# Optimization experiments

Hardware: AMD Instinct MI355X
Metric: run time of the kernel (lower is better)

Reference implementation:

```python
import jax, jax.numpy as jnp
import numpy as np
import math

B, S, H, D = 2, 2048, 12, 64
DIM = H * D
TOTAL = B * S


def setup_inputs() -> dict:
    key = jax.random.key(0)
    ks = jax.random.split(key, 5)
    hidden_states = jax.random.normal(ks[0], (TOTAL, DIM), dtype=jnp.float32)
    Wqkv_w = jax.random.normal(ks[1], (3 * DIM, DIM), dtype=jnp.float32) * (1.0 / math.sqrt(DIM))
    Wqkv_b = jax.random.normal(ks[2], (3 * DIM,), dtype=jnp.float32) * 0.02
    bias = jax.random.normal(ks[3], (B, H, S, S), dtype=jnp.float32) * 0.1
    slopes = jax.random.uniform(ks[4], (H,), dtype=jnp.float32)
    cu_seqlens = jnp.array([0, S, 2 * S], dtype=jnp.int32)
    indices = jnp.arange(TOTAL, dtype=jnp.int64)
    attn_mask = jnp.ones((B, S), dtype=jnp.int32)
    return {"hidden_states": hidden_states, "Wqkv_w": Wqkv_w, "Wqkv_b": Wqkv_b,
            "bias": bias, "slopes": slopes, "cu_seqlens": cu_seqlens,
            "indices": indices, "attn_mask": attn_mask, "max_seqlen": S}


def reference(hidden_states, Wqkv_w, Wqkv_b, bias, slopes, cu_seqlens, indices, attn_mask, max_seqlen):
    total_nnz, dim = hidden_states.shape
    batch = cu_seqlens.shape[0] - 1
    # fused QKV projection (torch Linear: x @ W.T + b)
    qkv = hidden_states @ Wqkv_w.T + Wqkv_b  # (total_nnz, 3*dim)
    # pad_input: scatter unpadded rows into (batch*max_seqlen, 3*dim)
    padded = jnp.zeros((batch * max_seqlen, 3 * dim), dtype=qkv.dtype).at[indices].set(qkv)
    qkv = padded.reshape(batch, max_seqlen, 3, H, D)
    q = qkv[:, :, 0].transpose(0, 2, 1, 3)  # (b, h, s, d)
    k = qkv[:, :, 1].transpose(0, 2, 1, 3)
    v = qkv[:, :, 2].transpose(0, 2, 1, 3)
    scores = jnp.einsum('bhqd,bhkd->bhqk', q, k) / math.sqrt(D)
    scores = scores + bias  # ALiBi (dense bias tensor)
    probs = jax.nn.softmax(scores, axis=-1)  # dropout p=0 -> identity
    attn = jnp.einsum('bhqk,bhkd->bhqd', probs, v)
    attn = attn.transpose(0, 2, 1, 3).reshape(batch * max_seqlen, dim)
    # unpad_input_only: gather valid rows back
    return attn[indices]
```

## Files before the change

kernel.cpp:

```cpp
#include <hip/hip_runtime.h>


typedef __attribute__((ext_vector_type(8))) short short8;
typedef __attribute__((ext_vector_type(4))) float floatx4;
typedef unsigned short u16;
typedef unsigned int u32;

#define LOG2E 1.4426950408889634f

__device__ __forceinline__ u16 f2bf(float f) {
  u32 u = __float_as_uint(f);
  u += 0x7FFFu + ((u >> 16) & 1u);
  return (u16)(u >> 16);
}

typedef const __attribute__((address_space(1))) u32* gp_t;
typedef __attribute__((address_space(3))) u32* lp_t;
__device__ __forceinline__ void async_cp16(const void* g, void* l) {
  __builtin_amdgcn_global_load_lds((gp_t)g, (lp_t)l, 16, 0, 0);
}

__global__ __launch_bounds__(256) void pack_kernel(
    const float* __restrict__ A, const float* __restrict__ W,
    u16* __restrict__ Abf, u16* __restrict__ Wbf) {
  unsigned u = blockIdx.x * 256u + threadIdx.x;
  const unsigned nA = 786432u;
  float4 v;
  u16* dst;
  if (u < nA) { v = ((const float4*)A)[u]; dst = Abf + u * 4; }
  else        { unsigned q = u - nA; v = ((const float4*)W)[q]; dst = Wbf + q * 4; }
  ushort4 o;
  o.x = f2bf(v.x); o.y = f2bf(v.y); o.z = f2bf(v.z); o.w = f2bf(v.w);
  *(ushort4*)dst = o;
}

__global__ __launch_bounds__(256, 3) void qkv_gemm(
    const u16* __restrict__ Abf, const u16* __restrict__ Wbf,
    const float* __restrict__ bq,
    u16* __restrict__ Qb, u16* __restrict__ Kb, u16* __restrict__ Vb) {
  __shared__ __align__(16) char smem[32768];
  char* As0 = smem;
  char* Bs0 = smem + 8192;
  char* As1 = smem + 16384;
  char* Bs1 = smem + 24576;
  const unsigned t = threadIdx.x;
  unsigned orig = blockIdx.y * 18u + blockIdx.x;
  unsigned wg = (orig & 7u) * 72u + (orig >> 3);
  const unsigned nblk = wg % 18u, mblk = wg / 18u;
  const unsigned w = t >> 6, l = t & 63, quad = l >> 4, c = l & 15;
  const unsigned wm = (w >> 1) * 64, wn = (w & 1) * 64;

  floatx4 acc[4][4] = {};

  const unsigned b0 = t, b1 = t + 256u;
  const unsigned r0 = b0 >> 2, ch0 = (b0 & 3u) ^ (r0 & 3u);
  const unsigned r1 = b1 >> 2, ch1 = (b1 & 3u) ^ (r1 & 3u);
  const char* gA0 = (const char*)Abf + (size_t)((mblk * 128 + r0) * 768) * 2 + ch0 * 16;
  const char* gA1 = (const char*)Abf + (size_t)((mblk * 128 + r1) * 768) * 2 + ch1 * 16;
  const char* gB0 = (const char*)Wbf + (size_t)((nblk * 128 + r0) * 768) * 2 + ch0 * 16;
  const char* gB1 = (const char*)Wbf + (size_t)((nblk * 128 + r1) * 768) * 2 + ch1 * 16;

  async_cp16(gA0, As0 + b0 * 16);
  async_cp16(gA1, As0 + b1 * 16);
  async_cp16(gB0, Bs0 + b0 * 16);
  async_cp16(gB1, Bs0 + b1 * 16);
  __syncthreads();

  for (unsigned kt = 0; kt < 24; ++kt) {
    char* Ac = (kt & 1u) ? As1 : As0;
    char* Bc = (kt & 1u) ? Bs1 : Bs0;
    if (kt + 1 < 24) {
      char* An = (kt & 1u) ? As0 : As1;
      char* Bn = (kt & 1u) ? Bs0 : Bs1;
      async_cp16(gA0 + (kt + 1) * 64, An + b0 * 16);
      async_cp16(gA1 + (kt + 1) * 64, An + b1 * 16);
      async_cp16(gB0 + (kt + 1) * 64, Bn + b0 * 16);
      async_cp16(gB1 + (kt + 1) * 64, Bn + b1 * 16);
    }
    short8 af[4], bf[4];
#pragma unroll
    for (int mt = 0; mt < 4; ++mt) {
      unsigned row = wm + mt * 16 + c;
      af[mt] = *(const short8*)(Ac + row * 64 + 16 * (quad ^ (row & 3u)));
    }
#pragma unroll
    for (int nt = 0; nt < 4; ++nt) {
      unsigned row = wn + nt * 16 + c;
      bf[nt] = *(const short8*)(Bc + row * 64 + 16 * (quad ^ (row & 3u)));
    }
#pragma unroll
    for (int mt = 0; mt < 4; ++mt)
#pragma unroll
      for (int nt = 0; nt < 4; ++nt)
        acc[mt][nt] = __builtin_amdgcn_mfma_f32_16x16x32_bf16(af[mt], bf[nt], acc[mt][nt], 0, 0, 0);
    __syncthreads();
  }

  float bqv[4];
#pragma unroll
  for (int nt = 0; nt < 4; ++nt) bqv[nt] = bq[nblk * 128 + wn + nt * 16 + c];
#pragma unroll
  for (int mt = 0; mt < 4; ++mt) {
#pragma unroll
    for (int r = 0; r < 4; ++r) {
      unsigned m = mblk * 128 + wm + mt * 16 + quad * 4 + r;
      unsigned bb = m >> 11, s = m & 2047u;
#pragma unroll
      for (int nt = 0; nt < 4; ++nt) {
        float val = acc[mt][nt][r] + bqv[nt];
        unsigned n = nblk * 128 + wn + nt * 16 + c;
        u16 bv = f2bf(val);
        if (n < 768u) {
          unsigned h = n >> 6, d = n & 63u;
          Qb[(((bb * 12 + h) * 2048 + s) << 6) + d] = bv;
        } else if (n < 1536u) {
          unsigned n2 = n - 768u, h = n2 >> 6, d = n2 & 63u;
          Kb[(((bb * 12 + h) * 2048 + s) << 6) + d] = bv;
        } else {
          unsigned n2 = n - 1536u, h = n2 >> 6, d = n2 & 63u;
          Vb[(((bb * 12 + h) << 6) + d) * 2048 + s] = bv;
        }
      }
    }
  }
}

__global__ __launch_bounds__(256, 6) void attn_kernel(
    const u16* __restrict__ Qb, const u16* __restrict__ Kb,
    const u16* __restrict__ Vb, const float* __restrict__ bias,
    float* __restrict__ Op, float* __restrict__ Mp, float* __restrict__ Lp) {
  __shared__ __align__(16) char smem[20480];
  char* Ks0 = smem;
  char* Ks1 = smem + 4096;
  char* Vs0 = smem + 8192;
  char* Vs1 = smem + 12288;
  char* Ps  = smem + 16384;
  const unsigned t = threadIdx.x;
  unsigned wgid = (blockIdx.x & 7u) * 384u + (blockIdx.x >> 3);
  const unsigned bh = wgid >> 7;
  const unsigned rem = wgid & 127u;
  const unsigned qt = rem >> 2, sp = rem & 3u;
  const unsigned q0 = qt * 64;
  const unsigned w = t >> 6, l = t & 63, quad = l >> 4, c = l & 15;

  const unsigned rK = t >> 3, chK = (t & 7u) ^ (rK & 7u);
  const unsigned rV = t >> 2, chV = (t & 3u) ^ (rV & 3u);

  const char* gK = (const char*)Kb + (size_t)(bh * 2048 + sp * 512 + rK) * 128 + chK * 16;
  const char* gV = (const char*)Vb + (size_t)(bh * 64 + rV) * 4096 + sp * 1024 + chV * 16;
  const float* bias_base = bias + (size_t)(bh * 2048 + q0 + w * 16 + quad * 4) * 2048
                                + sp * 512 + c;
  const unsigned pb = w * 1024u;

  async_cp16(gK, Ks0 + t * 16);
  async_cp16(gV, Vs0 + t * 16);
  short8 aq[2];
  {
    const u16* qrow = Qb + (size_t)(bh * 2048 + q0 + w * 16 + c) * 64 + quad * 8;
    aq[0] = *(const short8*)(qrow);
    aq[1] = *(const short8*)(qrow + 32);
  }
  float bvA[2][4], bvB[2][4];
#pragma unroll
  for (int tt = 0; tt < 2; ++tt)
#pragma unroll
    for (int r = 0; r < 4; ++r)
      bvA[tt][r] = bias_base[(size_t)r * 2048 + tt * 16];
  __syncthreads();

  float mrun[4] = {-1e30f, -1e30f, -1e30f, -1e30f};
  float lrun[4] = {0.f, 0.f, 0.f, 0.f};
  floatx4 oacc[4] = {};

  for (unsigned i = 0; i < 16; ++i) {
    const char* Kc = (i & 1u) ? Ks1 : Ks0;
    const char* Vc = (i & 1u) ? Vs1 : Vs0;

    if (i + 1 < 16) {
      char* Kn = (i & 1u) ? Ks0 : Ks1;
      char* Vn = (i & 1u) ? Vs0 : Vs1;
      async_cp16(gK + (size_t)(i + 1) * 4096, Kn + t * 16);
      async_cp16(gV + (size_t)(i + 1) * 64, Vn + t * 16);
#pragma unroll
      for (int tt = 0; tt < 2; ++tt)
#pragma unroll
        for (int r = 0; r < 4; ++r)
          bvB[tt][r] = bias_base[(size_t)r * 2048 + (i + 1) * 32 + tt * 16];
    }

    floatx4 s4[2] = {};
    __builtin_amdgcn_s_setprio(1);
#pragma unroll
    for (int ds = 0; ds < 2; ++ds)
#pragma unroll
      for (int tt = 0; tt < 2; ++tt) {
        unsigned row = tt * 16 + c;
        short8 kf = *(const short8*)(Kc + row * 128 + 16 * (((unsigned)quad + 4u * ds) ^ (c & 7u)));
        s4[tt] = __builtin_amdgcn_mfma_f32_16x16x32_bf16(aq[ds], kf, s4[tt], 0, 0, 0);
      }
    __builtin_amdgcn_s_setprio(0);

    float alpha[4];
    float pr[2][4];
#pragma unroll
    for (int r = 0; r < 4; ++r) {
      float x0 = fmaf(bvA[0][r], 8.0f, s4[0][r]) * (LOG2E / 8.0f);
      float x1 = fmaf(bvA[1][r], 8.0f, s4[1][r]) * (LOG2E / 8.0f);
      float mx = fmaxf(x0, x1);
      mx = fmaxf(mx, __shfl_xor(mx, 1));
      mx = fmaxf(mx, __shfl_xor(mx, 2));
      mx = fmaxf(mx, __shfl_xor(mx, 4));
      mx = fmaxf(mx, __shfl_xor(mx, 8));
      float mn = fmaxf(mrun[r], mx);
      float a = __builtin_amdgcn_exp2f(mrun[r] - mn);
      mrun[r] = mn;
      float p0 = __builtin_amdgcn_exp2f(x0 - mn);
      float p1 = __builtin_amdgcn_exp2f(x1 - mn);
      pr[0][r] = p0; pr[1][r] = p1;
      float rs = p0 + p1;
      rs += __shfl_xor(rs, 1);
      rs += __shfl_xor(rs, 2);
      rs += __shfl_xor(rs, 4);
      rs += __shfl_xor(rs, 8);
      lrun[r] = lrun[r] * a + rs;
      alpha[r] = a;
    }
#pragma unroll
    for (int dt = 0; dt < 4; ++dt) {
      oacc[dt][0] *= alpha[0]; oacc[dt][1] *= alpha[1];
      oacc[dt][2] *= alpha[2]; oacc[dt][3] *= alpha[3];
    }

#pragma unroll
    for (int tt = 0; tt < 2; ++tt)
#pragma unroll
      for (int r = 0; r < 4; ++r) {
        unsigned qq = quad * 4 + r;
        unsigned off = pb + qq * 64 + 16 * (((unsigned)(2 * tt) + (c >> 3)) ^ (qq & 3u)) + 2 * (c & 7u);
        *(u16*)(Ps + off) = f2bf(pr[tt][r]);
      }
    asm volatile("s_waitcnt lgkmcnt(0)" ::: "memory");

    __builtin_amdgcn_s_setprio(1);
    {
      short8 pf = *(const short8*)(Ps + pb + (l & 15) * 64 + 16 * ((unsigned)quad ^ ((l & 15) & 3u)));
#pragma unroll
      for (int dt = 0; dt < 4; ++dt) {
        unsigned row = dt * 16 + c;
        short8 vf = *(const short8*)(Vc + row * 64 + 16 * ((unsigned)quad ^ (c & 3u)));
        oacc[dt] = __builtin_amdgcn_mfma_f32_16x16x32_bf16(pf, vf, oacc[dt], 0, 0, 0);
      }
    }
    __builtin_amdgcn_s_setprio(0);

    __syncthreads();

    if (i + 1 < 16) {
#pragma unroll
      for (int tt = 0; tt < 2; ++tt)
#pragma unroll
        for (int r = 0; r < 4; ++r)
          bvA[tt][r] = bvB[tt][r];
    }
  }

  const unsigned pidx = (bh * 32u + qt) * 4u + sp;
#pragma unroll
  for (int r = 0; r < 4; ++r) {
    unsigned row = w * 16 + quad * 4 + r;
    float* op = Op + (size_t)pidx * 4096 + row * 64 + c;
#pragma unroll
    for (int dt = 0; dt < 4; ++dt) op[dt * 16] = oacc[dt][r];
    if (c == 0) {
      Mp[pidx * 64 + row] = mrun[r];
      Lp[pidx * 64 + row] = lrun[r];
    }
  }
}

__global__ __launch_bounds__(256) void combine_kernel(
    const float* __restrict__ Op, const float* __restrict__ Mp,
    const float* __restrict__ Lp, float* __restrict__ out) {
  unsigned gid = blockIdx.x * 256u + threadIdx.x;
  unsigned d = gid & 63u;
  unsigned row = gid >> 6;
  unsigned bh = row >> 11, q = row & 2047u;
  unsigned qt = q >> 6, qr = q & 63u;
  unsigned pidx0 = (bh * 32u + qt) * 4u;
  size_t ob = (size_t)pidx0 * 4096 + qr * 64u + d;
  unsigned mb = pidx0 * 64u + qr;
  float m0 = Mp[mb], m1 = Mp[mb + 64], m2 = Mp[mb + 128], m3 = Mp[mb + 192];
  float ms = fmaxf(fmaxf(m0, m1), fmaxf(m2, m3));
  float w0 = __builtin_amdgcn_exp2f(m0 - ms);
  float w1 = __builtin_amdgcn_exp2f(m1 - ms);
  float w2 = __builtin_amdgcn_exp2f(m2 - ms);
  float w3 = __builtin_amdgcn_exp2f(m3 - ms);
  float den = w0 * Lp[mb] + w1 * Lp[mb + 64] + w2 * Lp[mb + 128] + w3 * Lp[mb + 192];
  float num = w0 * Op[ob] + w1 * Op[ob + 4096] + w2 * Op[ob + 8192] + w3 * Op[ob + 12288];
  unsigned b_ = bh / 12u, h = bh - b_ * 12u;
  out[(size_t)(b_ * 2048 + q) * 768 + h * 64 + d] = num / den;
}

extern "C" void kernel_launch(void* const* d_in, const int* in_sizes, int n_in,
                              void* d_out, int out_size, void* d_ws, size_t ws_size,
                              hipStream_t stream) {
  const float* hidden = (const float*)d_in[0];
  const float* Wqkv_w = (const float*)d_in[1];
  const float* Wqkv_b = (const float*)d_in[2];
  const float* bias   = (const float*)d_in[3];
  float* out = (float*)d_out;

  char* ws = (char*)d_ws;
  u16* Abf = (u16*)(ws);
  u16* Wbf = (u16*)(ws + 6291456);
  u16* Qb  = (u16*)(ws + 9830400);
  u16* Kb  = (u16*)(ws + 16121856);
  u16* Vb  = (u16*)(ws + 22413312);
  float* Op = (float*)(ws + 28704768);
  float* Mp = (float*)(ws + 79036416);
  float* Lp = (float*)(ws + 79822848);

  pack_kernel<<<4800, 256, 0, stream>>>(hidden, Wqkv_w, Abf, Wbf);
  qkv_gemm<<<dim3(18, 32), 256, 0, stream>>>(Abf, Wbf, Wqkv_b, Qb, Kb, Vb);
  attn_kernel<<<3072, 256, 0, stream>>>(Qb, Kb, Vb, bias, Op, Mp, Lp);
  combine_kernel<<<12288, 256, 0, stream>>>(Op, Mp, Lp, out);
}
```

Baseline: 645.6 us.

## Load K/V fragments directly from global, drop LDS staging and barriers

The attention kernel no longer stages K and V tiles through double-buffered LDS with async copies and block barriers. Each wave now reads its K and V MFMA fragments straight from global memory (relying on L1/L2 reuse across the four waves), and the key tile per iteration doubles from 32 to 64 with the P buffer grown to match. This removes __syncthreads and LDS traffic and halves the loop trip count, at the cost of four times more global load requests per block, no software prefetch of the next tile's bias or K/V, and exposed global-load latency each iteration.

```diff
diff --git a/kernel.cpp b/kernel.cpp
--- a/kernel.cpp
+++ b/kernel.cpp
@@ -129,12 +129,8 @@
     const u16* __restrict__ Qb, const u16* __restrict__ Kb,
     const u16* __restrict__ Vb, const float* __restrict__ bias,
     float* __restrict__ Op, float* __restrict__ Mp, float* __restrict__ Lp) {
-  __shared__ __align__(16) char smem[20480];
-  char* Ks0 = smem;
-  char* Ks1 = smem + 4096;
-  char* Vs0 = smem + 8192;
-  char* Vs1 = smem + 12288;
-  char* Ps  = smem + 16384;
+  __shared__ __align__(16) char smem[8192];
+  char* Ps = smem;
   const unsigned t = threadIdx.x;
   unsigned wgid = (blockIdx.x & 7u) * 384u + (blockIdx.x >> 3);
   const unsigned bh = wgid >> 7;
@@ -142,71 +138,56 @@
   const unsigned qt = rem >> 2, sp = rem & 3u;
   const unsigned q0 = qt * 64;
   const unsigned w = t >> 6, l = t & 63, quad = l >> 4, c = l & 15;
-
-  const unsigned rK = t >> 3, chK = (t & 7u) ^ (rK & 7u);
-  const unsigned rV = t >> 2, chV = (t & 3u) ^ (rV & 3u);
-
-  const char* gK = (const char*)Kb + (size_t)(bh * 2048 + sp * 512 + rK) * 128 + chK * 16;
-  const char* gV = (const char*)Vb + (size_t)(bh * 64 + rV) * 4096 + sp * 1024 + chV * 16;
-  const float* bias_base = bias + (size_t)(bh * 2048 + q0 + w * 16 + quad * 4) * 2048
-                                + sp * 512 + c;
-  const unsigned pb = w * 1024u;
-
-  async_cp16(gK, Ks0 + t * 16);
-  async_cp16(gV, Vs0 + t * 16);
+  const unsigned pb = w * 2048u;
+
   short8 aq[2];
   {
     const u16* qrow = Qb + (size_t)(bh * 2048 + q0 + w * 16 + c) * 64 + quad * 8;
     aq[0] = *(const short8*)(qrow);
     aq[1] = *(const short8*)(qrow + 32);
   }
-  float bvA[2][4], bvB[2][4];
-#pragma unroll
-  for (int tt = 0; tt < 2; ++tt)
-#pragma unroll
-    for (int r = 0; r < 4; ++r)
-      bvA[tt][r] = bias_base[(size_t)r * 2048 + tt * 16];
-  __syncthreads();
+
+  const char* gKt = (const char*)Kb + (size_t)(bh * 2048 + sp * 512 + c) * 128 + quad * 16;
+  const char* gVt = (const char*)Vb + (size_t)(bh * 64 + c) * 4096 + sp * 1024 + quad * 16;
+  const float* bias_base = bias + (size_t)(bh * 2048 + q0 + w * 16 + quad * 4) * 2048
+                                + sp * 512 + c;
 
   float mrun[4] = {-1e30f, -1e30f, -1e30f, -1e30f};
   float lrun[4] = {0.f, 0.f, 0.f, 0.f};
   floatx4 oacc[4] = {};
 
-  for (unsigned i = 0; i < 16; ++i) {
-    const char* Kc = (i & 1u) ? Ks1 : Ks0;
-    const char* Vc = (i & 1u) ? Vs1 : Vs0;
-
-    if (i + 1 < 16) {
-      char* Kn = (i & 1u) ? Ks0 : Ks1;
-      char* Vn = (i & 1u) ? Vs0 : Vs1;
-      async_cp16(gK + (size_t)(i + 1) * 4096, Kn + t * 16);
-      async_cp16(gV + (size_t)(i + 1) * 64, Vn + t * 16);
-#pragma unroll
-      for (int tt = 0; tt < 2; ++tt)
-#pragma unroll
-        for (int r = 0; r < 4; ++r)
-          bvB[tt][r] = bias_base[(size_t)r * 2048 + (i + 1) * 32 + tt * 16];
-    }
-
-    floatx4 s4[2] = {};
-    __builtin_amdgcn_s_setprio(1);
-#pragma unroll
-    for (int ds = 0; ds < 2; ++ds)
-#pragma unroll
-      for (int tt = 0; tt < 2; ++tt) {
-        unsigned row = tt * 16 + c;
-        short8 kf = *(const short8*)(Kc + row * 128 + 16 * (((unsigned)quad + 4u * ds) ^ (c & 7u)));
-        s4[tt] = __builtin_amdgcn_mfma_f32_16x16x32_bf16(aq[ds], kf, s4[tt], 0, 0, 0);
-      }
-    __builtin_amdgcn_s_setprio(0);
+  for (unsigned i = 0; i < 8; ++i) {
+    float bv[4][4];
+#pragma unroll
+    for (int tt = 0; tt < 4; ++tt)
+#pragma unroll
+      for (int r = 0; r < 4; ++r)
+        bv[tt][r] = bias_base[(size_t)r * 2048 + i * 64 + tt * 16];
+
+    floatx4 s4[4] = {};
+#pragma unroll
+    for (int ds = 0; ds < 2; ++ds) {
+      short8 kf[4];
+#pragma unroll
+      for (int tt = 0; tt < 4; ++tt)
+        kf[tt] = *(const short8*)(gKt + (size_t)i * 8192 + tt * 2048 + ds * 64);
+      __builtin_amdgcn_s_setprio(1);
+#pragma unroll
+      for (int tt = 0; tt < 4; ++tt)
+        s4[tt] = __builtin_amdgcn_mfma_f32_16x16x32_bf16(aq[ds], kf[tt], s4[tt], 0, 0, 0);
+      __builtin_amdgcn_s_setprio(0);
+    }
+
+#pragma unroll
+    for (int tt = 0; tt < 4; ++tt)
+#pragma unroll
+      for (int r = 0; r < 4; ++r)
+        s4[tt][r] = fmaf(bv[tt][r], 8.0f, s4[tt][r]) * (LOG2E / 8.0f);
 
     float alpha[4];
-    float pr[2][4];
 #pragma unroll
     for (int r = 0; r < 4; ++r) {
-      float x0 = fmaf(bvA[0][r], 8.0f, s4[0][r]) * (LOG2E / 8.0f);
-      float x1 = fmaf(bvA[1][r], 8.0f, s4[1][r]) * (LOG2E / 8.0f);
-      float mx = fmaxf(x0, x1);
+      float mx = fmaxf(fmaxf(s4[0][r], s4[1][r]), fmaxf(s4[2][r], s4[3][r]));
       mx = fmaxf(mx, __shfl_xor(mx, 1));
       mx = fmaxf(mx, __shfl_xor(mx, 2));
       mx = fmaxf(mx, __shfl_xor(mx, 4));
@@ -214,10 +195,12 @@
       float mn = fmaxf(mrun[r], mx);
       float a = __builtin_amdgcn_exp2f(mrun[r] - mn);
       mrun[r] = mn;
-      float p0 = __builtin_amdgcn_exp2f(x0 - mn);
-      float p1 = __builtin_amdgcn_exp2f(x1 - mn);
-      pr[0][r] = p0; pr[1][r] = p1;
-      float rs = p0 + p1;
+      float p0 = __builtin_amdgcn_exp2f(s4[0][r] - mn);
+      float p1 = __builtin_amdgcn_exp2f(s4[1][r] - mn);
+      float p2 = __builtin_amdgcn_exp2f(s4[2][r] - mn);
+      float p3 = __builtin_amdgcn_exp2f(s4[3][r] - mn);
+      s4[0][r] = p0; s4[1][r] = p1; s4[2][r] = p2; s4[3][r] = p3;
+      float rs = (p0 + p1) + (p2 + p3);
       rs += __shfl_xor(rs, 1);
       rs += __shfl_xor(rs, 2);
       rs += __shfl_xor(rs, 4);
@@ -232,35 +215,28 @@
     }
 
 #pragma unroll
-    for (int tt = 0; tt < 2; ++tt)
+    for (int tt = 0; tt < 4; ++tt)
 #pragma unroll
       for (int r = 0; r < 4; ++r) {
         unsigned qq = quad * 4 + r;
-        unsigned off = pb + qq * 64 + 16 * (((unsigned)(2 * tt) + (c >> 3)) ^ (qq & 3u)) + 2 * (c & 7u);
-        *(u16*)(Ps + off) = f2bf(pr[tt][r]);
+        unsigned off = pb + qq * 128 + 16 * (((unsigned)(2 * tt) + (c >> 3)) ^ (qq & 7u)) + 2 * (c & 7u);
+        *(u16*)(Ps + off) = f2bf(s4[tt][r]);
       }
     asm volatile("s_waitcnt lgkmcnt(0)" ::: "memory");
 
-    __builtin_amdgcn_s_setprio(1);
-    {
-      short8 pf = *(const short8*)(Ps + pb + (l & 15) * 64 + 16 * ((unsigned)quad ^ ((l & 15) & 3u)));
-#pragma unroll
-      for (int dt = 0; dt < 4; ++dt) {
-        unsigned row = dt * 16 + c;
-        short8 vf = *(const short8*)(Vc + row * 64 + 16 * ((unsigned)quad ^ (c & 3u)));
-        oacc[dt] = __builtin_amdgcn_mfma_f32_16x16x32_bf16(pf, vf, oacc[dt], 0, 0, 0);
-      }
-    }
-    __builtin_amdgcn_s_setprio(0);
-
-    __syncthreads();
-
-    if (i + 1 < 16) {
-#pragma unroll
-      for (int tt = 0; tt < 2; ++tt)
-#pragma unroll
-        for (int r = 0; r < 4; ++r)
-          bvA[tt][r] = bvB[tt][r];
+#pragma unroll
+    for (int js = 0; js < 2; ++js) {
+      short8 pf = *(const short8*)(Ps + pb + (l & 15) * 128 +
+                                   16 * (((unsigned)quad + 4u * js) ^ ((l & 15) & 7u)));
+      short8 vf[4];
+#pragma unroll
+      for (int dt = 0; dt < 4; ++dt)
+        vf[dt] = *(const short8*)(gVt + (size_t)dt * 65536 + i * 128 + js * 64);
+      __builtin_amdgcn_s_setprio(1);
+#pragma unroll
+      for (int dt = 0; dt < 4; ++dt)
+        oacc[dt] = __builtin_amdgcn_mfma_f32_16x16x32_bf16(pf, vf[dt], oacc[dt], 0, 0, 0);
+      __builtin_amdgcn_s_setprio(0);
     }
   }
 
```

Result: slower. 857.5 us (+32.8%).

## Widen attention KV tile to 64, halve split-K, skip rescale when max unchanged

Applied to the files above, without the earlier changes.

The attention kernel now processes 64 keys per iteration instead of 32 and splits the key range two ways instead of four. That halves the workgroup count, the partial outputs written, and the work in the combine kernel. It also adds a wave-uniform check that skips the exp/rescale of the accumulators when no row max increased. Shared memory doubles to 40KB and launch bounds drop to 4 blocks per CU, which lowers occupancy, and the bias stream per workgroup becomes twice as long.

```diff
diff --git a/kernel.cpp b/kernel.cpp
--- a/kernel.cpp
+++ b/kernel.cpp
@@ -125,44 +125,49 @@
   }
 }
 
-__global__ __launch_bounds__(256, 6) void attn_kernel(
+__global__ __launch_bounds__(256, 4) void attn_kernel(
     const u16* __restrict__ Qb, const u16* __restrict__ Kb,
     const u16* __restrict__ Vb, const float* __restrict__ bias,
     float* __restrict__ Op, float* __restrict__ Mp, float* __restrict__ Lp) {
-  __shared__ __align__(16) char smem[20480];
+  __shared__ __align__(16) char smem[40960];
   char* Ks0 = smem;
-  char* Ks1 = smem + 4096;
-  char* Vs0 = smem + 8192;
-  char* Vs1 = smem + 12288;
-  char* Ps  = smem + 16384;
+  char* Ks1 = smem + 8192;
+  char* Vs0 = smem + 16384;
+  char* Vs1 = smem + 24576;
+  char* Ps  = smem + 32768;
   const unsigned t = threadIdx.x;
-  unsigned wgid = (blockIdx.x & 7u) * 384u + (blockIdx.x >> 3);
-  const unsigned bh = wgid >> 7;
-  const unsigned rem = wgid & 127u;
-  const unsigned qt = rem >> 2, sp = rem & 3u;
+  unsigned wgid = (blockIdx.x & 7u) * 192u + (blockIdx.x >> 3);
+  const unsigned bh = wgid >> 6;
+  const unsigned rem = wgid & 63u;
+  const unsigned qt = rem >> 1, sp = rem & 1u;
   const unsigned q0 = qt * 64;
   const unsigned w = t >> 6, l = t & 63, quad = l >> 4, c = l & 15;
-
-  const unsigned rK = t >> 3, chK = (t & 7u) ^ (rK & 7u);
-  const unsigned rV = t >> 2, chV = (t & 3u) ^ (rV & 3u);
-
-  const char* gK = (const char*)Kb + (size_t)(bh * 2048 + sp * 512 + rK) * 128 + chK * 16;
-  const char* gV = (const char*)Vb + (size_t)(bh * 64 + rV) * 4096 + sp * 1024 + chV * 16;
+  const unsigned pb = w * 2048u;
+
+  const unsigned b0 = t, b1 = t + 256u;
+  const unsigned r0 = b0 >> 3, ch0 = (b0 & 7u) ^ (r0 & 7u);
+  const unsigned r1 = b1 >> 3, ch1 = (b1 & 7u) ^ (r1 & 7u);
+
+  const char* gK0 = (const char*)Kb + (size_t)(bh * 2048 + sp * 1024 + r0) * 128 + ch0 * 16;
+  const char* gK1 = (const char*)Kb + (size_t)(bh * 2048 + sp * 1024 + r1) * 128 + ch1 * 16;
+  const char* gV0 = (const char*)Vb + (size_t)(bh * 64 + r0) * 4096 + sp * 2048 + ch0 * 16;
+  const char* gV1 = (const char*)Vb + (size_t)(bh * 64 + r1) * 4096 + sp * 2048 + ch1 * 16;
   const float* bias_base = bias + (size_t)(bh * 2048 + q0 + w * 16 + quad * 4) * 2048
-                                + sp * 512 + c;
-  const unsigned pb = w * 1024u;
-
-  async_cp16(gK, Ks0 + t * 16);
-  async_cp16(gV, Vs0 + t * 16);
+                                + sp * 1024 + c;
+
+  async_cp16(gK0, Ks0 + b0 * 16);
+  async_cp16(gK1, Ks0 + b1 * 16);
+  async_cp16(gV0, Vs0 + b0 * 16);
+  async_cp16(gV1, Vs0 + b1 * 16);
   short8 aq[2];
   {
     const u16* qrow = Qb + (size_t)(bh * 2048 + q0 + w * 16 + c) * 64 + quad * 8;
     aq[0] = *(const short8*)(qrow);
     aq[1] = *(const short8*)(qrow + 32);
   }
-  float bvA[2][4], bvB[2][4];
-#pragma unroll
-  for (int tt = 0; tt < 2; ++tt)
+  float bvA[4][4], bvB[4][4];
+#pragma unroll
+  for (int tt = 0; tt < 4; ++tt)
 #pragma unroll
     for (int r = 0; r < 4; ++r)
       bvA[tt][r] = bias_base[(size_t)r * 2048 + tt * 16];
@@ -173,81 +178,99 @@
   floatx4 oacc[4] = {};
 
   for (unsigned i = 0; i < 16; ++i) {
+    const unsigned k0 = i * 64u;
     const char* Kc = (i & 1u) ? Ks1 : Ks0;
     const char* Vc = (i & 1u) ? Vs1 : Vs0;
 
     if (i + 1 < 16) {
       char* Kn = (i & 1u) ? Ks0 : Ks1;
       char* Vn = (i & 1u) ? Vs0 : Vs1;
-      async_cp16(gK + (size_t)(i + 1) * 4096, Kn + t * 16);
-      async_cp16(gV + (size_t)(i + 1) * 64, Vn + t * 16);
-#pragma unroll
-      for (int tt = 0; tt < 2; ++tt)
+      async_cp16(gK0 + (size_t)(k0 + 64) * 128, Kn + b0 * 16);
+      async_cp16(gK1 + (size_t)(k0 + 64) * 128, Kn + b1 * 16);
+      async_cp16(gV0 + (size_t)(k0 + 64) * 2, Vn + b0 * 16);
+      async_cp16(gV1 + (size_t)(k0 + 64) * 2, Vn + b1 * 16);
+#pragma unroll
+      for (int tt = 0; tt < 4; ++tt)
 #pragma unroll
         for (int r = 0; r < 4; ++r)
-          bvB[tt][r] = bias_base[(size_t)r * 2048 + (i + 1) * 32 + tt * 16];
-    }
-
-    floatx4 s4[2] = {};
+          bvB[tt][r] = bias_base[(size_t)r * 2048 + (k0 + 64) + tt * 16];
+    }
+
+    floatx4 s4[4] = {};
     __builtin_amdgcn_s_setprio(1);
 #pragma unroll
     for (int ds = 0; ds < 2; ++ds)
 #pragma unroll
-      for (int tt = 0; tt < 2; ++tt) {
+      for (int tt = 0; tt < 4; ++tt) {
         unsigned row = tt * 16 + c;
         short8 kf = *(const short8*)(Kc + row * 128 + 16 * (((unsigned)quad + 4u * ds) ^ (c & 7u)));
         s4[tt] = __builtin_amdgcn_mfma_f32_16x16x32_bf16(aq[ds], kf, s4[tt], 0, 0, 0);
       }
     __builtin_amdgcn_s_setprio(0);
 
-    float alpha[4];
-    float pr[2][4];
+    float xv[4][4];
+    float mx4[4];
 #pragma unroll
     for (int r = 0; r < 4; ++r) {
-      float x0 = fmaf(bvA[0][r], 8.0f, s4[0][r]) * (LOG2E / 8.0f);
-      float x1 = fmaf(bvA[1][r], 8.0f, s4[1][r]) * (LOG2E / 8.0f);
-      float mx = fmaxf(x0, x1);
+      xv[0][r] = fmaf(bvA[0][r], 8.0f, s4[0][r]) * (LOG2E / 8.0f);
+      xv[1][r] = fmaf(bvA[1][r], 8.0f, s4[1][r]) * (LOG2E / 8.0f);
+      xv[2][r] = fmaf(bvA[2][r], 8.0f, s4[2][r]) * (LOG2E / 8.0f);
+      xv[3][r] = fmaf(bvA[3][r], 8.0f, s4[3][r]) * (LOG2E / 8.0f);
+      float mx = fmaxf(fmaxf(xv[0][r], xv[1][r]), fmaxf(xv[2][r], xv[3][r]));
       mx = fmaxf(mx, __shfl_xor(mx, 1));
       mx = fmaxf(mx, __shfl_xor(mx, 2));
       mx = fmaxf(mx, __shfl_xor(mx, 4));
       mx = fmaxf(mx, __shfl_xor(mx, 8));
-      float mn = fmaxf(mrun[r], mx);
-      float a = __builtin_amdgcn_exp2f(mrun[r] - mn);
-      mrun[r] = mn;
-      float p0 = __builtin_amdgcn_exp2f(x0 - mn);
-      float p1 = __builtin_amdgcn_exp2f(x1 - mn);
-      pr[0][r] = p0; pr[1][r] = p1;
-      float rs = p0 + p1;
+      mx4[r] = mx;
+    }
+    bool nochg = (mx4[0] <= mrun[0]) & (mx4[1] <= mrun[1]) &
+                 (mx4[2] <= mrun[2]) & (mx4[3] <= mrun[3]);
+    if (!__all(nochg)) {
+#pragma unroll
+      for (int r = 0; r < 4; ++r) {
+        float mn = fmaxf(mrun[r], mx4[r]);
+        float a = __builtin_amdgcn_exp2f(mrun[r] - mn);
+        mrun[r] = mn;
+        lrun[r] *= a;
+#pragma unroll
+        for (int dt = 0; dt < 4; ++dt) oacc[dt][r] *= a;
+      }
+    }
+    float pr[4][4];
+#pragma unroll
+    for (int r = 0; r < 4; ++r) {
+      float p0 = __builtin_amdgcn_exp2f(xv[0][r] - mrun[r]);
+      float p1 = __builtin_amdgcn_exp2f(xv[1][r] - mrun[r]);
+      float p2 = __builtin_amdgcn_exp2f(xv[2][r] - mrun[r]);
+      float p3 = __builtin_amdgcn_exp2f(xv[3][r] - mrun[r]);
+      pr[0][r] = p0; pr[1][r] = p1; pr[2][r] = p2; pr[3][r] = p3;
+      float rs = (p0 + p1) + (p2 + p3);
       rs += __shfl_xor(rs, 1);
       rs += __shfl_xor(rs, 2);
       rs += __shfl_xor(rs, 4);
       rs += __shfl_xor(rs, 8);
-      lrun[r] = lrun[r] * a + rs;
-      alpha[r] = a;
-    }
-#pragma unroll
-    for (int dt = 0; dt < 4; ++dt) {
-      oacc[dt][0] *= alpha[0]; oacc[dt][1] *= alpha[1];
-      oacc[dt][2] *= alpha[2]; oacc[dt][3] *= alpha[3];
-    }
-
-#pragma unroll
-    for (int tt = 0; tt < 2; ++tt)
+      lrun[r] += rs;
+    }
+
+#pragma unroll
+    for (int tt = 0; tt < 4; ++tt)
 #pragma unroll
       for (int r = 0; r < 4; ++r) {
         unsigned qq = quad * 4 + r;
-        unsigned off = pb + qq * 64 + 16 * (((unsigned)(2 * tt) + (c >> 3)) ^ (qq & 3u)) + 2 * (c & 7u);
+        unsigned off = pb + qq * 128 + 16 * (((unsigned)(2 * tt) + (c >> 3)) ^ (qq & 7u)) + 2 * (c & 7u);
         *(u16*)(Ps + off) = f2bf(pr[tt][r]);
       }
     asm volatile("s_waitcnt lgkmcnt(0)" ::: "memory");
 
     __builtin_amdgcn_s_setprio(1);
-    {
-      short8 pf = *(const short8*)(Ps + pb + (l & 15) * 64 + 16 * ((unsigned)quad ^ ((l & 15) & 3u)));
+#pragma unroll
+    for (int js = 0; js < 2; ++js) {
+      short8 pf = *(const short8*)(Ps + pb + (l & 15) * 128 +
+                                   16 * (((unsigned)quad + 4u * js) ^ ((l & 15) & 7u)));
 #pragma unroll
       for (int dt = 0; dt < 4; ++dt) {
         unsigned row = dt * 16 + c;
-        short8 vf = *(const short8*)(Vc + row * 64 + 16 * ((unsigned)quad ^ (c & 3u)));
+        short8 vf = *(const short8*)(Vc + row * 128 + 16 * (((unsigned)quad + 4u * js) ^ (c & 7u)));
         oacc[dt] = __builtin_amdgcn_mfma_f32_16x16x32_bf16(pf, vf, oacc[dt], 0, 0, 0);
       }
     }
@@ -257,14 +280,14 @@
 
     if (i + 1 < 16) {
 #pragma unroll
-      for (int tt = 0; tt < 2; ++tt)
+      for (int tt = 0; tt < 4; ++tt)
 #pragma unroll
         for (int r = 0; r < 4; ++r)
           bvA[tt][r] = bvB[tt][r];
     }
   }
 
-  const unsigned pidx = (bh * 32u + qt) * 4u + sp;
+  const unsigned pidx = (bh * 32u + qt) * 2u + sp;
 #pragma unroll
   for (int r = 0; r < 4; ++r) {
     unsigned row = w * 16 + quad * 4 + r;
@@ -286,17 +309,15 @@
   unsigned row = gid >> 6;
   unsigned bh = row >> 11, q = row & 2047u;
   unsigned qt = q >> 6, qr = q & 63u;
-  unsigned pidx0 = (bh * 32u + qt) * 4u;
+  unsigned pidx0 = (bh * 32u + qt) * 2u;
   size_t ob = (size_t)pidx0 * 4096 + qr * 64u + d;
   unsigned mb = pidx0 * 64u + qr;
-  float m0 = Mp[mb], m1 = Mp[mb + 64], m2 = Mp[mb + 128], m3 = Mp[mb + 192];
-  float ms = fmaxf(fmaxf(m0, m1), fmaxf(m2, m3));
+  float m0 = Mp[mb], m1 = Mp[mb + 64];
+  float ms = fmaxf(m0, m1);
   float w0 = __builtin_amdgcn_exp2f(m0 - ms);
   float w1 = __builtin_amdgcn_exp2f(m1 - ms);
-  float w2 = __builtin_amdgcn_exp2f(m2 - ms);
-  float w3 = __builtin_amdgcn_exp2f(m3 - ms);
-  float den = w0 * Lp[mb] + w1 * Lp[mb + 64] + w2 * Lp[mb + 128] + w3 * Lp[mb + 192];
-  float num = w0 * Op[ob] + w1 * Op[ob + 4096] + w2 * Op[ob + 8192] + w3 * Op[ob + 12288];
+  float den = w0 * Lp[mb] + w1 * Lp[mb + 64];
+  float num = w0 * Op[ob] + w1 * Op[ob + 4096];
   unsigned b_ = bh / 12u, h = bh - b_ * 12u;
   out[(size_t)(b_ * 2048 + q) * 768 + h * 64 + d] = num / den;
 }
@@ -317,11 +338,11 @@
   u16* Kb  = (u16*)(ws + 16121856);
   u16* Vb  = (u16*)(ws + 22413312);
   float* Op = (float*)(ws + 28704768);
-  float* Mp = (float*)(ws + 79036416);
-  float* Lp = (float*)(ws + 79822848);
+  float* Mp = (float*)(ws + 53870592);
+  float* Lp = (float*)(ws + 54263808);
 
   pack_kernel<<<4800, 256, 0, stream>>>(hidden, Wqkv_w, Abf, Wbf);
   qkv_gemm<<<dim3(18, 32), 256, 0, stream>>>(Abf, Wbf, Wqkv_b, Qb, Kb, Vb);
-  attn_kernel<<<3072, 256, 0, stream>>>(Qb, Kb, Vb, bias, Op, Mp, Lp);
+  attn_kernel<<<1536, 256, 0, stream>>>(Qb, Kb, Vb, bias, Op, Mp, Lp);
   combine_kernel<<<12288, 256, 0, stream>>>(Op, Mp, Lp, out);
 }
```

New measurement: 644.9 us. About the same (-0.1%).
